# Optimization experiments

Hardware: AMD Instinct MI355X
Metric: run time of the kernel (lower is better)

Reference implementation:

```python
import jax, jax.numpy as jnp
import numpy as np

# Dims (match init_kwargs)
B, S, D = 2, 2048, 2048
H = 16
Q_LORA, KV_LORA = 768, 512
NOPE, ROPE, VD = 128, 64, 128
QHD = NOPE + ROPE  # 192


def setup_inputs() -> dict:
    key = jax.random.key(0)
    ks = jax.random.split(key, 7)
    w = lambda k, shape: (jax.random.normal(k, shape, jnp.float32) * 0.02)
    return {
        "x": jax.random.normal(ks[0], (B, S, D), jnp.float32),
        "position": jnp.broadcast_to(jnp.arange(S, dtype=jnp.int32), (B, S)),
        "mask": jnp.tril(jnp.ones((1, 1, S, S), jnp.int32)),  # causal
        "w_q_down": w(ks[1], (D, Q_LORA)),                 # (in, out) layout
        "w_q_up": w(ks[2], (Q_LORA, H * QHD)),
        "w_kv_down": w(ks[3], (D, KV_LORA + ROPE)),
        "w_kv_up": w(ks[4], (KV_LORA, H * (NOPE + VD))),
        "w_out": w(ks[5], (H * VD, D)),
    }


def reference(x, position, mask, w_q_down, w_q_up, w_kv_down, w_kv_up, w_out):
    # position unused: rope_embedding is None in the source module.
    # Low-rank Q: down then up projection.
    q = (x @ w_q_down) @ w_q_up                      # [B,S,H*QHD]
    q = q.reshape(B, S, H, QHD).transpose(0, 2, 1, 3)  # [B,H,S,QHD]
    q_nope, q_rope = q[..., :NOPE], q[..., NOPE:]

    # Low-rank KV: down projection yields compressed kv + shared rope key.
    c = x @ w_kv_down                                # [B,S,KV_LORA+ROPE]
    c_kv, k_rope = c[..., :KV_LORA], c[..., KV_LORA:]
    k_rope = k_rope[:, None, :, :]                   # [B,1,S,ROPE]

    kv = (c_kv @ w_kv_up).reshape(B, S, H, NOPE + VD).transpose(0, 2, 1, 3)
    k_nope, v = kv[..., :NOPE], kv[..., NOPE:]       # [B,H,S,NOPE], [B,H,S,VD]

    q_state = jnp.concatenate([q_nope, q_rope], axis=-1)           # [B,H,S,QHD]
    k_state = jnp.concatenate(
        [k_nope, jnp.broadcast_to(k_rope, (B, H, S, ROPE))], axis=-1)

    scale = 1.0 / jnp.sqrt(jnp.float32(VD))  # source divides by sqrt(v_head_dim)
    scores = jnp.einsum("bhqd,bhkd->bhqk", q_state, k_state) * scale
    scores = jnp.where(mask == 0, jnp.float32(-jnp.inf), scores)
    att = jax.nn.softmax(scores, axis=-1)            # dropout_rate=0 (eval)
    out = jnp.einsum("bhqk,bhkd->bhqd", att, v)      # [B,H,S,VD]
    out = out.transpose(0, 2, 1, 3).reshape(B, S, H * VD)
    return out @ w_out
```

## Files before the change

kernel.cpp:

```cpp
#include <hip/hip_runtime.h>

typedef __bf16 bf16;
typedef bf16 bf16x8 __attribute__((ext_vector_type(8)));
typedef bf16 bf16x4 __attribute__((ext_vector_type(4)));
typedef float f32x4 __attribute__((ext_vector_type(4)));
typedef short s16x4 __attribute__((ext_vector_type(4)));

#define AS1 __attribute__((address_space(1)))
#define AS3 __attribute__((address_space(3)))

__device__ __forceinline__ void load_lds16(const void* g, void* l) {
    __builtin_amdgcn_global_load_lds((const AS1 unsigned int*)g,
                                     (AS3 unsigned int*)l, 16, 0, 0);
}

__device__ __forceinline__ void tc_body(
        const float* __restrict__ in, bf16* __restrict__ out,
        int K, int N, int Np, int bx, int by, int tid,
        float (*tile)[33]) {
    const int tx = tid & 31, ty = tid >> 5;
#pragma unroll
    for (int i = 0; i < 4; ++i) {
        int k = by + ty + i * 8, n = bx + tx;
        float v = (k < K && n < N) ? in[(size_t)k * N + n] : 0.f;
        tile[ty + i * 8][tx] = v;
    }
    __syncthreads();
#pragma unroll
    for (int i = 0; i < 4; ++i) {
        int n = bx + ty + i * 8, k = by + tx;
        if (n < Np && k < K) out[(size_t)n * K + k] = (bf16)tile[tx][ty + i * 8];
    }
}

__global__ __launch_bounds__(256) void prep_fused(
        const float* __restrict__ x,    bf16* __restrict__ xb,
        const float* __restrict__ wqd,  bf16* __restrict__ wqdT,
        const float* __restrict__ wkvd, bf16* __restrict__ wkvdT,
        const float* __restrict__ wqu,  bf16* __restrict__ wquT,
        const float* __restrict__ wkvu, bf16* __restrict__ wkvuT,
        const float* __restrict__ wout, bf16* __restrict__ woutT) {
    __shared__ float tile[32][33];
    const int tid = threadIdx.x;
    int r = blockIdx.x;
    if (r < 8192) {
        int i = (r * 256 + tid) * 4;
        float4 v = *(const float4*)(x + i);
        bf16x4 o = { (bf16)v.x, (bf16)v.y, (bf16)v.z, (bf16)v.w };
        *(bf16x4*)(xb + i) = o;
        return;
    }
    r -= 8192;
    if (r < 1536) { tc_body(wqd,  wqdT,  2048, 768,  768,  (r % 24) * 32, (r / 24) * 32, tid, tile); return; }
    r -= 1536;
    if (r < 1280) { tc_body(wkvd, wkvdT, 2048, 576,  640,  (r % 20) * 32, (r / 20) * 32, tid, tile); return; }
    r -= 1280;
    if (r < 2304) { tc_body(wqu,  wquT,  768,  3072, 3072, (r % 96) * 32, (r / 96) * 32, tid, tile); return; }
    r -= 2304;
    if (r < 2048) { tc_body(wkvu, wkvuT, 512,  4096, 4096, (r % 128) * 32, (r / 128) * 32, tid, tile); return; }
    r -= 2048;
    tc_body(wout, woutT, 2048, 2048, 2048, (r % 64) * 32, (r / 64) * 32, tid, tile);
}

__device__ __forceinline__ void gemm_acc(
        const bf16* __restrict__ A, const bf16* __restrict__ Bt,
        int K, int lda, int ldb, int m0, int n0,
        bf16* As, bf16* Bs, f32x4 acc[4][4]) {
    const int tid = threadIdx.x;
    const int wave = tid >> 6, lane = tid & 63;
    const int l15 = lane & 15, quad = lane >> 4;
    const int wm = (wave >> 1) * 64, wn = (wave & 1) * 64;

    for (int k0 = 0; k0 < K; k0 += 64) {
#pragma unroll
        for (int c = 0; c < 4; ++c) {
            int e = wave * 2048 + c * 512 + lane * 8;
            int r = e >> 6, col = e & 63;
            load_lds16(A + (size_t)(m0 + r) * lda + k0 + col,
                       &As[wave * 2048 + c * 512]);
            load_lds16(Bt + (size_t)(n0 + r) * ldb + k0 + col,
                       &Bs[wave * 2048 + c * 512]);
        }
        __syncthreads();
#pragma unroll
        for (int kk = 0; kk < 64; kk += 32) {
            bf16x8 af[4], bf[4];
#pragma unroll
            for (int i = 0; i < 4; ++i)
                af[i] = *(const bf16x8*)&As[(wm + i * 16 + l15) * 64 + kk + quad * 8];
#pragma unroll
            for (int j = 0; j < 4; ++j)
                bf[j] = *(const bf16x8*)&Bs[(wn + j * 16 + l15) * 64 + kk + quad * 8];
#pragma unroll
            for (int i = 0; i < 4; ++i)
#pragma unroll
                for (int j = 0; j < 4; ++j)
                    acc[i][j] = __builtin_amdgcn_mfma_f32_16x16x32_bf16(
                        af[i], bf[j], acc[i][j], 0, 0, 0);
        }
        __syncthreads();
    }
}

template <typename OutT>
__device__ __forceinline__ void store_c(
        f32x4 acc[4][4], OutT* __restrict__ C, int ldc, int m0, int n0) {
    const int tid = threadIdx.x;
    const int wave = tid >> 6, lane = tid & 63;
    const int l15 = lane & 15, quad = lane >> 4;
    const int wm = (wave >> 1) * 64, wn = (wave & 1) * 64;
#pragma unroll
    for (int i = 0; i < 4; ++i)
#pragma unroll
        for (int j = 0; j < 4; ++j) {
            int row = m0 + wm + i * 16 + quad * 4;
            int col = n0 + wn + j * 16 + l15;
#pragma unroll
            for (int r = 0; r < 4; ++r)
                C[(size_t)(row + r) * ldc + col] = (OutT)acc[i][j][r];
        }
}

template <typename OutT>
__global__ __launch_bounds__(256) void gemm_bt(
        const bf16* __restrict__ A, const bf16* __restrict__ Bt,
        OutT* __restrict__ C, int K, int lda, int ldb, int ldc) {
    __shared__ __align__(16) bf16 As[128 * 64];
    __shared__ __align__(16) bf16 Bs[128 * 64];
    f32x4 acc[4][4] = {};
    gemm_acc(A, Bt, K, lda, ldb, blockIdx.y * 128, blockIdx.x * 128, As, Bs, acc);
    store_c<OutT>(acc, C, ldc, blockIdx.y * 128, blockIdx.x * 128);
}

__global__ __launch_bounds__(256) void gemm_up(
        const bf16* __restrict__ qd, const bf16* __restrict__ wquT,
        bf16* __restrict__ qb,
        const bf16* __restrict__ cb, const bf16* __restrict__ wkvuT,
        bf16* __restrict__ kvb, bf16* __restrict__ vtb) {
    __shared__ __align__(16) bf16 shbuf[2 * 128 * 64];
    bf16* As = shbuf;
    bf16* Bs = shbuf + 128 * 64;
    f32x4 acc[4][4] = {};
    const int m0 = blockIdx.y * 128;
    if (blockIdx.x < 24) {
        const int n0 = blockIdx.x * 128;
        gemm_acc(qd, wquT, 768, 768, 768, m0, n0, As, Bs, acc);
        store_c<bf16>(acc, qb, 3072, m0, n0);
        return;
    }
    const int n0 = (blockIdx.x - 24) * 128;
    gemm_acc(cb, wkvuT, 512, 640, 512, m0, n0, As, Bs, acc);
    if ((n0 & 255) == 0) {
        store_c<bf16>(acc, kvb, 4096, m0, n0);
        return;
    }
    const int tid = threadIdx.x;
    const int wave = tid >> 6, lane = tid & 63;
    const int l15 = lane & 15, quad = lane >> 4;
    const int wm = (wave >> 1) * 64, wn = (wave & 1) * 64;
    const int h = n0 >> 8;
    const int bb = m0 >> 11;
    const int kvbase = m0 & 2047;
    bf16* vt = vtb + (size_t)((bb * 16 + h) * 128) * 2048;
    bf16* t = shbuf;
#pragma unroll
    for (int p = 0; p < 2; ++p) {
        if ((wn >> 6) == p) {
#pragma unroll
            for (int i = 0; i < 4; ++i)
#pragma unroll
                for (int j = 0; j < 4; ++j) {
                    bf16x4 v;
#pragma unroll
                    for (int r = 0; r < 4; ++r) v[r] = (bf16)acc[i][j][r];
                    const int colL = j * 16 + l15;
                    const int row = wm + i * 16 + quad * 4;
                    *(bf16x4*)&t[colL * 136 + row] = v;
                }
        }
        __syncthreads();
        {
            const int vd = tid >> 2;
            const int kvo = (tid & 3) * 32;
#pragma unroll
            for (int u = 0; u < 4; ++u) {
                bf16x8 vv = *(const bf16x8*)&t[vd * 136 + kvo + u * 8];
                *(bf16x8*)&vt[(size_t)(p * 64 + vd) * 2048 + kvbase + kvo + u * 8] = vv;
            }
        }
        __syncthreads();
    }
}

__global__ __launch_bounds__(256) void gemm_down(
        const bf16* __restrict__ A, const bf16* __restrict__ Bt,
        bf16* __restrict__ C1, bf16* __restrict__ C2) {
    __shared__ __align__(16) bf16 As[128 * 64];
    __shared__ __align__(16) bf16 Bs[128 * 64];
    f32x4 acc[4][4] = {};
    const int n0 = blockIdx.x * 128, m0 = blockIdx.y * 128;
    gemm_acc(A, Bt, 2048, 2048, 2048, m0, n0, As, Bs, acc);
    if (n0 < 768) store_c<bf16>(acc, C1, 768, m0, n0);
    else          store_c<bf16>(acc, C2, 640, m0, n0 - 768);
}

__global__ __launch_bounds__(1024, 4) void mla_attention_split(
        const bf16* __restrict__ qb, const bf16* __restrict__ kvb,
        const bf16* __restrict__ cb, const bf16* __restrict__ vtb,
        bf16* __restrict__ ob, bf16* __restrict__ part_o,
        float* __restrict__ part_ml) {
    constexpr int S = 2048;
    const signed char k_of[20]  = {7,7,7,7, 6,6,6,6, 5,5,5, 4,4,4, 3,3, 2,2, 1, 0};
    const signed char c_of[20]  = {0,1,2,3, 0,1,2,3, 0,1,2, 0,1,2, 0,1, 0,1, 0, 0};
    const signed char np_of[8]  = {1,1,2,2,3,3,4,4};
    const signed char pre_of[8] = {0,0,0,1,2,4,6,9};

    const int k  = k_of[blockIdx.x], c = c_of[blockIdx.x];
    const int np = np_of[k];
    const int h = blockIdx.y, b = blockIdx.z;
    const int T  = 4 * k + 4;
    const int t0 = (c * T) / np, t1 = ((c + 1) * T) / np;
    const int q0 = k * 256;

    const int tid = threadIdx.x, wave = tid >> 6, lane = tid & 63;
    const int l15 = lane & 15, quad = lane >> 4;

    __shared__ __align__(16) bf16 Ks[2][24 * 512];
    __shared__ __align__(16) bf16 Vs[2][8 * 1024];

    const int qrow = q0 + wave * 16 + l15;
    bf16x8 qf[6];
    {
        const bf16* qr = qb + (size_t)(b * S + qrow) * 3072 + h * 192;
#pragma unroll
        for (int ks = 0; ks < 6; ++ks)
            qf[ks] = *(const bf16x8*)(qr + ks * 32 + quad * 8);
    }

    const bf16* vt_head = vtb + (size_t)((b * 16 + h) * 128) * 2048;

    auto stage = [&](int kt, int bufi) {
        const int kv0 = kt * 64;
        if (wave < 8) {
            const int mt = wave >> 1;
            const size_t row = (size_t)(b * S + kv0 + mt * 16 + l15);
#pragma unroll
            for (int i = 0; i < 3; ++i) {
                const int ks = (wave & 1) * 3 + i;
                const bf16* g = (ks < 4)
                    ? kvb + row * 4096 + h * 256 + ks * 32 + quad * 8
                    : cb  + row * 640  + 512 + (ks - 4) * 32 + quad * 8;
                load_lds16(g, &Ks[bufi][(mt * 6 + ks) * 512]);
            }
        } else {
            const int nt = wave - 8;
#pragma unroll
            for (int i = 0; i < 2; ++i) {
                const bf16* g = vt_head + (size_t)(nt * 16 + l15) * 2048
                                + kv0 + (i * 4 + quad) * 8;
                load_lds16(g, &Vs[bufi][nt * 1024 + i * 512]);
            }
        }
    };

    f32x4 o[8] = {};
    float m_i = -1e30f, l_i = 0.f;
    const float sm_scale = 0.08838834764831845f * 1.4426950408889634f;
    const int qmin_w = q0 + wave * 16;

    stage(t0, 0);
    stage(t0 + 1, 1);

    int cur = 0;
    for (int kt = t0; kt < t1; ++kt, cur ^= 1) {
        const int kv0 = kt * 64;

        if (kt + 1 < t1) {
            if (wave < 8) asm volatile("s_waitcnt vmcnt(3)" ::: "memory");
            else          asm volatile("s_waitcnt vmcnt(2)" ::: "memory");
        } else {
            asm volatile("s_waitcnt vmcnt(0)" ::: "memory");
        }
        __builtin_amdgcn_s_barrier();
        __builtin_amdgcn_sched_barrier(0);

        f32x4 s[4];
        __builtin_amdgcn_s_setprio(1);
#pragma unroll
        for (int mt = 0; mt < 4; ++mt) {
            f32x4 a = {};
#pragma unroll
            for (int ks = 0; ks < 6; ++ks) {
                bf16x8 kf = *(const bf16x8*)&Ks[cur][(mt * 6 + ks) * 512 + lane * 8];
                a = __builtin_amdgcn_mfma_f32_16x16x32_bf16(kf, qf[ks], a, 0, 0, 0);
            }
            s[mt] = a;
        }
        __builtin_amdgcn_s_setprio(0);

        if (kv0 + 63 > qmin_w) {
#pragma unroll
            for (int mt = 0; mt < 4; ++mt)
#pragma unroll
                for (int r = 0; r < 4; ++r) {
                    int kvi = kv0 + mt * 16 + quad * 4 + r;
                    s[mt][r] = (kvi <= qrow) ? s[mt][r] * sm_scale : -1e30f;
                }
        } else {
#pragma unroll
            for (int mt = 0; mt < 4; ++mt)
#pragma unroll
                for (int r = 0; r < 4; ++r)
                    s[mt][r] = s[mt][r] * sm_scale;
        }
        float mx4[4];
#pragma unroll
        for (int mt = 0; mt < 4; ++mt)
            mx4[mt] = fmaxf(fmaxf(s[mt][0], s[mt][1]),
                            fmaxf(s[mt][2], s[mt][3]));
        float mx = fmaxf(fmaxf(mx4[0], mx4[1]), fmaxf(mx4[2], mx4[3]));
        mx = fmaxf(mx, __shfl_xor(mx, 16, 64));
        mx = fmaxf(mx, __shfl_xor(mx, 32, 64));
        float m_new = fmaxf(m_i, mx);
        float su4[4];
        bf16x4 pf[4];
#pragma unroll
        for (int mt = 0; mt < 4; ++mt) {
            float e0 = exp2f(s[mt][0] - m_new);
            float e1 = exp2f(s[mt][1] - m_new);
            float e2 = exp2f(s[mt][2] - m_new);
            float e3 = exp2f(s[mt][3] - m_new);
            su4[mt] = (e0 + e1) + (e2 + e3);
            pf[mt][0] = (bf16)e0; pf[mt][1] = (bf16)e1;
            pf[mt][2] = (bf16)e2; pf[mt][3] = (bf16)e3;
        }
        float su = (su4[0] + su4[1]) + (su4[2] + su4[3]);
        su += __shfl_xor(su, 16, 64);
        su += __shfl_xor(su, 32, 64);
        if (__all(mx <= m_i)) {
            l_i += su;
        } else {
            float alpha = exp2f(m_i - m_new);
            l_i = l_i * alpha + su;
            m_i = m_new;
            float alpha_r[4];
#pragma unroll
            for (int r = 0; r < 4; ++r)
                alpha_r[r] = __shfl(alpha, quad * 4 + r, 64);
#pragma unroll
            for (int nt = 0; nt < 8; ++nt)
#pragma unroll
                for (int r = 0; r < 4; ++r) o[nt][r] *= alpha_r[r];
        }

        __builtin_amdgcn_s_setprio(1);
#pragma unroll
        for (int ktk = 0; ktk < 4; ++ktk) {
            s16x4 a = __builtin_bit_cast(s16x4, pf[ktk]);
            const int voff = ktk * 256 + (quad >> 1) * 128 + l15 * 8 + (quad & 1) * 4;
#pragma unroll
            for (int nt = 0; nt < 8; ++nt) {
                s16x4 bfv = __builtin_bit_cast(s16x4,
                    *(const bf16x4*)&Vs[cur][nt * 1024 + voff]);
                o[nt] = __builtin_amdgcn_mfma_f32_16x16x16bf16_1k(a, bfv, o[nt], 0, 0, 0);
            }
        }
        __builtin_amdgcn_s_setprio(0);

        __builtin_amdgcn_s_barrier();
        if (kt + 2 < t1) stage(kt + 2, cur);
    }

    if (np == 1) {
        float l_r[4];
#pragma unroll
        for (int r = 0; r < 4; ++r) l_r[r] = __shfl(l_i, quad * 4 + r, 64);
        bf16* obase = ob + (size_t)(b * S + q0 + wave * 16) * 2048 + h * 128;
#pragma unroll
        for (int nt = 0; nt < 8; ++nt)
#pragma unroll
            for (int r = 0; r < 4; ++r)
                obase[(size_t)(quad * 4 + r) * 2048 + nt * 16 + l15] =
                    (bf16)(o[nt][r] / l_r[r]);
    } else {
        const int bh = b * 16 + h;
        if (quad == 0) {
            const int qlocal = wave * 16 + l15;
            float* mlp = part_ml + ((size_t)(bh * 8 + k) * 4 + c) * 512;
            mlp[qlocal] = m_i;
            mlp[256 + qlocal] = l_i;
        }
        if (c == np - 1) {
            bf16* obase = ob + (size_t)(b * S + q0 + wave * 16) * 2048 + h * 128;
#pragma unroll
            for (int nt = 0; nt < 8; ++nt)
#pragma unroll
                for (int r = 0; r < 4; ++r)
                    obase[(size_t)(quad * 4 + r) * 2048 + nt * 16 + l15] =
                        (bf16)o[nt][r];
        } else {
            bf16* pb = part_o + (size_t)(bh * 12 + pre_of[k] + c) * 32768
                       + (size_t)(wave * 16) * 128;
#pragma unroll
            for (int nt = 0; nt < 8; ++nt)
#pragma unroll
                for (int r = 0; r < 4; ++r)
                    pb[(quad * 4 + r) * 128 + nt * 16 + l15] = (bf16)o[nt][r];
        }
    }
}

__global__ __launch_bounds__(256) void mla_merge(
        const bf16* __restrict__ part_o, const float* __restrict__ part_ml,
        bf16* __restrict__ ob) {
    const signed char np_of[8]  = {1,1,2,2,3,3,4,4};
    const signed char pre_of[8] = {0,0,0,1,2,4,6,9};
    const int k = 2 + blockIdx.x;
    const int h = blockIdx.y, b = blockIdx.z;
    const int bh = b * 16 + h;
    const int np = np_of[k];
    const int row = threadIdx.x;

    const float* mlb = part_ml + (size_t)(bh * 8 + k) * 4 * 512;
    const float m0 = mlb[row],            l0 = mlb[256 + row];
    const float m1 = mlb[512 + row],      l1 = mlb[512 + 256 + row];
    const float m2 = (np > 2) ? mlb[1024 + row] : -1e30f;
    const float l2 = (np > 2) ? mlb[1024 + 256 + row] : 0.f;
    const float m3 = (np > 3) ? mlb[1536 + row] : -1e30f;
    const float l3 = (np > 3) ? mlb[1536 + 256 + row] : 0.f;
    const float M = fmaxf(fmaxf(m0, m1), fmaxf(m2, m3));
    float a0 = exp2f(m0 - M), a1 = exp2f(m1 - M);
    float a2 = exp2f(m2 - M), a3 = exp2f(m3 - M);
    const float inv = 1.f / (l0 * a0 + l1 * a1 + l2 * a2 + l3 * a3);
    a0 *= inv; a1 *= inv; a2 *= inv; a3 *= inv;
    const float alast = (np == 2) ? a1 : (np == 3) ? a2 : a3;

    const bf16* p0 = part_o + (size_t)(bh * 12 + pre_of[k]) * 32768 + row * 128;
    const bf16* p1 = p0 + 32768;
    const bf16* p2 = p1 + 32768;
    bf16* po = ob + (size_t)(b * 2048 + k * 256 + row) * 2048 + h * 128;
#pragma unroll
    for (int i = 0; i < 16; ++i) {
        bf16x8 vb = *(const bf16x8*)(po + i * 8);
        bf16x8 v0 = *(const bf16x8*)(p0 + i * 8);
        float acc[8];
#pragma unroll
        for (int u = 0; u < 8; ++u)
            acc[u] = (float)vb[u] * alast + (float)v0[u] * a0;
        if (np > 2) {
            bf16x8 v1 = *(const bf16x8*)(p1 + i * 8);
#pragma unroll
            for (int u = 0; u < 8; ++u) acc[u] += (float)v1[u] * a1;
        }
        if (np > 3) {
            bf16x8 v2 = *(const bf16x8*)(p2 + i * 8);
#pragma unroll
            for (int u = 0; u < 8; ++u) acc[u] += (float)v2[u] * a2;
        }
        bf16x8 om;
#pragma unroll
        for (int u = 0; u < 8; ++u) om[u] = (bf16)acc[u];
        *(bf16x8*)(po + i * 8) = om;
    }
}

extern "C" void kernel_launch(void* const* d_in, const int* in_sizes, int n_in,
                              void* d_out, int out_size, void* d_ws, size_t ws_size,
                              hipStream_t stream) {
    const float* x    = (const float*)d_in[0];
    const float* wqd  = (const float*)d_in[3];
    const float* wqu  = (const float*)d_in[4];
    const float* wkvd = (const float*)d_in[5];
    const float* wkvu = (const float*)d_in[6];
    const float* wout = (const float*)d_in[7];
    float* out = (float*)d_out;
    char* ws = (char*)d_ws;

    bf16* xb    = (bf16*)(ws + 0);
    bf16* vtb   = (bf16*)(ws + 0);
    bf16* wqdT  = (bf16*)(ws + 16777216);
    bf16* wkvdT = (bf16*)(ws + 19922944);
    bf16* wquT  = (bf16*)(ws + 22544384);
    bf16* wkvuT = (bf16*)(ws + 27262976);
    float* part_ml = (float*)(ws + 16777216);
    bf16* part_o  = (bf16*)out;
    bf16* woutT = (bf16*)(ws + 31457280);
    bf16* qd    = (bf16*)(ws + 39845888);
    bf16* qb    = (bf16*)(ws + 46137344);
    bf16* cb    = (bf16*)(ws + 71303168);
    bf16* kvb   = (bf16*)(ws + 76546048);
    bf16* attnb = (bf16*)(ws + 110100480);

    prep_fused<<<19456, 256, 0, stream>>>(x, xb, wqd, wqdT, wkvd, wkvdT,
                                          wqu, wquT, wkvu, wkvuT, wout, woutT);

    gemm_down<<<dim3(11, 32), 256, 0, stream>>>(xb, wqdT, qd, cb);
    gemm_up<<<dim3(56, 32), 256, 0, stream>>>(qd, wquT, qb, cb, wkvuT, kvb, vtb);

    mla_attention_split<<<dim3(20, 16, 2), 1024, 0, stream>>>(
        qb, kvb, cb, vtb, attnb, part_o, part_ml);
    mla_merge<<<dim3(6, 16, 2), 256, 0, stream>>>(part_o, part_ml, attnb);

    gemm_bt<float><<<dim3(16, 32), 256, 0, stream>>>(attnb, woutT, out, 2048, 2048, 2048, 2048);
}
```

Baseline: 455.7 us.

## Replace up-projection GEMM with 256x256 double-buffered LDS-async tile kernel

The combined Q/KV up-projection GEMM now uses 256x256 output tiles with 512 threads, double-buffered global-to-LDS direct loads, an XOR-swizzled LDS layout and explicit barrier/priority scheduling around the MFMA loop. Each head's 256 KV columns are handled by one block, which writes k_nope directly and transposes V through LDS into the V^T buffer. The larger tiles give more data reuse per block and the prefetch overlaps loads with MFMA work. In exchange the grid is much smaller (448 blocks), the kernel uses 128 KB of LDS, and per-thread register use is high.

```diff
diff --git a/kernel.cpp b/kernel.cpp
--- a/kernel.cpp
+++ b/kernel.cpp
@@ -132,66 +132,6 @@
     store_c<OutT>(acc, C, ldc, blockIdx.y * 128, blockIdx.x * 128);
 }
 
-__global__ __launch_bounds__(256) void gemm_up(
-        const bf16* __restrict__ qd, const bf16* __restrict__ wquT,
-        bf16* __restrict__ qb,
-        const bf16* __restrict__ cb, const bf16* __restrict__ wkvuT,
-        bf16* __restrict__ kvb, bf16* __restrict__ vtb) {
-    __shared__ __align__(16) bf16 shbuf[2 * 128 * 64];
-    bf16* As = shbuf;
-    bf16* Bs = shbuf + 128 * 64;
-    f32x4 acc[4][4] = {};
-    const int m0 = blockIdx.y * 128;
-    if (blockIdx.x < 24) {
-        const int n0 = blockIdx.x * 128;
-        gemm_acc(qd, wquT, 768, 768, 768, m0, n0, As, Bs, acc);
-        store_c<bf16>(acc, qb, 3072, m0, n0);
-        return;
-    }
-    const int n0 = (blockIdx.x - 24) * 128;
-    gemm_acc(cb, wkvuT, 512, 640, 512, m0, n0, As, Bs, acc);
-    if ((n0 & 255) == 0) {
-        store_c<bf16>(acc, kvb, 4096, m0, n0);
-        return;
-    }
-    const int tid = threadIdx.x;
-    const int wave = tid >> 6, lane = tid & 63;
-    const int l15 = lane & 15, quad = lane >> 4;
-    const int wm = (wave >> 1) * 64, wn = (wave & 1) * 64;
-    const int h = n0 >> 8;
-    const int bb = m0 >> 11;
-    const int kvbase = m0 & 2047;
-    bf16* vt = vtb + (size_t)((bb * 16 + h) * 128) * 2048;
-    bf16* t = shbuf;
-#pragma unroll
-    for (int p = 0; p < 2; ++p) {
-        if ((wn >> 6) == p) {
-#pragma unroll
-            for (int i = 0; i < 4; ++i)
-#pragma unroll
-                for (int j = 0; j < 4; ++j) {
-                    bf16x4 v;
-#pragma unroll
-                    for (int r = 0; r < 4; ++r) v[r] = (bf16)acc[i][j][r];
-                    const int colL = j * 16 + l15;
-                    const int row = wm + i * 16 + quad * 4;
-                    *(bf16x4*)&t[colL * 136 + row] = v;
-                }
-        }
-        __syncthreads();
-        {
-            const int vd = tid >> 2;
-            const int kvo = (tid & 3) * 32;
-#pragma unroll
-            for (int u = 0; u < 4; ++u) {
-                bf16x8 vv = *(const bf16x8*)&t[vd * 136 + kvo + u * 8];
-                *(bf16x8*)&vt[(size_t)(p * 64 + vd) * 2048 + kvbase + kvo + u * 8] = vv;
-            }
-        }
-        __syncthreads();
-    }
-}
-
 __global__ __launch_bounds__(256) void gemm_down(
         const bf16* __restrict__ A, const bf16* __restrict__ Bt,
         bf16* __restrict__ C1, bf16* __restrict__ C2) {
@@ -202,6 +142,142 @@
     gemm_acc(A, Bt, 2048, 2048, 2048, m0, n0, As, Bs, acc);
     if (n0 < 768) store_c<bf16>(acc, C1, 768, m0, n0);
     else          store_c<bf16>(acc, C2, 640, m0, n0 - 768);
+}
+
+__global__ __launch_bounds__(512, 2) void gemm_up256(
+        const bf16* __restrict__ qd, const bf16* __restrict__ wquT,
+        bf16* __restrict__ qb,
+        const bf16* __restrict__ cb, const bf16* __restrict__ wkvuT,
+        bf16* __restrict__ kvb, bf16* __restrict__ vtb) {
+    __shared__ __align__(16) bf16 sh[65536];
+    const int tid = threadIdx.x;
+    const int wave = tid >> 6, lane = tid & 63;
+    const int l15 = lane & 15, quad = lane >> 4;
+    const int wr = wave >> 2, wc = wave & 3;
+    const int m0 = blockIdx.y * 256;
+    const bool is_q = blockIdx.x < 12;
+    const int n0 = is_q ? blockIdx.x * 256 : (blockIdx.x - 12) * 256;
+    const bf16* Ag  = is_q ? qd : cb;
+    const bf16* Btg = is_q ? wquT : wkvuT;
+    const int lda = is_q ? 768 : 640;
+    const int ldb = is_q ? 768 : 512;
+    const int NT  = is_q ? 12 : 8;
+
+    const int gcol = (((tid & 7) ^ ((tid >> 3) & 7)) * 8);
+    auto stage = [&](int kt, int bufi) {
+        const int k0 = kt * 64;
+#pragma unroll
+        for (int c = 0; c < 4; ++c) {
+            const int row = c * 64 + (tid >> 3);
+            const int ldsb = bufi * 16384 + c * 4096 + wave * 512;
+            load_lds16(Ag  + (size_t)(m0 + row) * lda + k0 + gcol, &sh[ldsb]);
+            load_lds16(Btg + (size_t)(n0 + row) * ldb + k0 + gcol, &sh[32768 + ldsb]);
+        }
+    };
+
+    const int sw = (l15 & 7) * 8;
+    f32x4 acc[8][4] = {};
+
+    stage(0, 0);
+    asm volatile("s_waitcnt vmcnt(0)" ::: "memory");
+    __builtin_amdgcn_s_barrier();
+    __builtin_amdgcn_sched_barrier(0);
+
+    for (int kt = 0; kt < NT; ++kt) {
+        const int bufi = kt & 1;
+        const bf16* As_ = &sh[bufi * 16384];
+        const bf16* Bs_ = &sh[32768 + bufi * 16384];
+        bf16x8 bfr[4][2];
+#pragma unroll
+        for (int p = 0; p < 4; ++p) {
+            bf16x8 afr[2][2];
+#pragma unroll
+            for (int ii = 0; ii < 2; ++ii) {
+                const int arow = (wr * 128 + (p * 2 + ii) * 16 + l15) * 64;
+#pragma unroll
+                for (int kki = 0; kki < 2; ++kki)
+                    afr[ii][kki] = *(const bf16x8*)&As_[arow + ((kki * 32 + quad * 8) ^ sw)];
+            }
+            if (p == 0) {
+#pragma unroll
+                for (int j = 0; j < 4; ++j) {
+                    const int brow = (wc * 64 + j * 16 + l15) * 64;
+#pragma unroll
+                    for (int kki = 0; kki < 2; ++kki)
+                        bfr[j][kki] = *(const bf16x8*)&Bs_[brow + ((kki * 32 + quad * 8) ^ sw)];
+                }
+                if (kt + 1 < NT) stage(kt + 1, bufi ^ 1);
+            }
+            __builtin_amdgcn_s_barrier();
+            asm volatile("s_waitcnt lgkmcnt(0)" ::: "memory");
+            __builtin_amdgcn_sched_barrier(0);
+            __builtin_amdgcn_s_setprio(1);
+#pragma unroll
+            for (int ii = 0; ii < 2; ++ii)
+#pragma unroll
+                for (int j = 0; j < 4; ++j)
+#pragma unroll
+                    for (int kki = 0; kki < 2; ++kki)
+                        acc[p * 2 + ii][j] = __builtin_amdgcn_mfma_f32_16x16x32_bf16(
+                            afr[ii][kki], bfr[j][kki], acc[p * 2 + ii][j], 0, 0, 0);
+            __builtin_amdgcn_s_setprio(0);
+            if (p == 3) asm volatile("s_waitcnt vmcnt(0)" ::: "memory");
+            __builtin_amdgcn_s_barrier();
+            __builtin_amdgcn_sched_barrier(0);
+        }
+    }
+
+    if (is_q) {
+#pragma unroll
+        for (int i = 0; i < 8; ++i)
+#pragma unroll
+            for (int j = 0; j < 4; ++j) {
+                const int row = m0 + wr * 128 + i * 16 + quad * 4;
+                const int col = n0 + wc * 64 + j * 16 + l15;
+#pragma unroll
+                for (int r = 0; r < 4; ++r)
+                    qb[(size_t)(row + r) * 3072 + col] = (bf16)acc[i][j][r];
+            }
+        return;
+    }
+    const int h = n0 >> 8;
+    const int bb = m0 >> 11, kvbase = m0 & 2047;
+    bf16* t = sh;
+    if (wc < 2) {
+#pragma unroll
+        for (int i = 0; i < 8; ++i)
+#pragma unroll
+            for (int j = 0; j < 4; ++j) {
+                const int row = m0 + wr * 128 + i * 16 + quad * 4;
+                const int col = h * 256 + wc * 64 + j * 16 + l15;
+#pragma unroll
+                for (int r = 0; r < 4; ++r)
+                    kvb[(size_t)(row + r) * 4096 + col] = (bf16)acc[i][j][r];
+            }
+    } else {
+#pragma unroll
+        for (int i = 0; i < 8; ++i)
+#pragma unroll
+            for (int j = 0; j < 4; ++j) {
+                const int vd = (wc - 2) * 64 + j * 16 + l15;
+                const int kv = wr * 128 + i * 16 + quad * 4;
+                bf16x4 v;
+#pragma unroll
+                for (int r = 0; r < 4; ++r) v[r] = (bf16)acc[i][j][r];
+                *(bf16x4*)&t[vd * 264 + kv] = v;
+            }
+    }
+    __syncthreads();
+    {
+        bf16* vt = vtb + (size_t)((bb * 16 + h) * 128) * 2048;
+        const int vd = tid >> 2;
+        const int kv4 = (tid & 3) * 64;
+#pragma unroll
+        for (int u = 0; u < 8; ++u) {
+            bf16x8 vv = *(const bf16x8*)&t[vd * 264 + kv4 + u * 8];
+            *(bf16x8*)&vt[(size_t)vd * 2048 + kvbase + kv4 + u * 8] = vv;
+        }
+    }
 }
 
 __global__ __launch_bounds__(1024, 4) void mla_attention_split(
@@ -495,7 +571,7 @@
                                           wqu, wquT, wkvu, wkvuT, wout, woutT);
 
     gemm_down<<<dim3(11, 32), 256, 0, stream>>>(xb, wqdT, qd, cb);
-    gemm_up<<<dim3(56, 32), 256, 0, stream>>>(qd, wquT, qb, cb, wkvuT, kvb, vtb);
+    gemm_up256<<<dim3(28, 16), 512, 0, stream>>>(qd, wquT, qb, cb, wkvuT, kvb, vtb);
 
     mla_attention_split<<<dim3(20, 16, 2), 1024, 0, stream>>>(
         qb, kvb, cb, vtb, attnb, part_o, part_ml);
```

New measurement: 442.0 us. -3.0%, faster.
